# Kernel optimization log

Hardware: AMD Instinct MI355X
Metric: run time of the kernel (lower is better)

## Reference

```python
import jax, jax.numpy as jnp
import numpy as np
from jax import lax

C_OUT, C_IN, KH, KW = 16, 16, 3, 3
STRIDE = (1, 1)
PADDING = ((1, 1), (1, 1))  # symmetric 'same' padding for 3x3, stride 1
DILATION = (1, 1)


def setup_inputs() -> dict:
    key = jax.random.key(0)
    kx, kw = jax.random.split(key)
    x = jax.random.normal(kx, (8, C_IN, 512, 512), dtype=jnp.float32)
    # Conv2DUF stores the conv weight flattened: [out_channels, in_channels*kh*kw]
    weight = jax.random.normal(kw, (C_OUT, C_IN * KH * KW), dtype=jnp.float32) * 0.1
    return {"x": x, "weight": weight}


def reference(x, weight):
    # forward(): F.conv2d(x, weight.reshape(original shape), stride/padding/dilation/groups)
    w = weight.reshape(C_OUT, C_IN, KH, KW)
    out = lax.conv_general_dilated(
        x, w,
        window_strides=STRIDE,
        padding=PADDING,
        rhs_dilation=DILATION,
        dimension_numbers=("NCHW", "OIHW", "NCHW"),
        feature_group_count=1,
    )
    return out  # [8, 16, 512, 512]
```

## Files before the change

kernel.cpp:

```cpp
#include <hip/hip_runtime.h>
#include <hip/hip_bf16.h>


#define IH 512
#define IW 512
#define CI 16
#define CO 16
#define TH 16
#define TW 64
#define LROWS (TH + 2)
#define LCOLS (TW + 2)

typedef short short8  __attribute__((ext_vector_type(8)));
typedef short short4v __attribute__((ext_vector_type(4)));
typedef float f32x4   __attribute__((ext_vector_type(4)));

__device__ __forceinline__ short f32_to_bf16_bits(float v) {
    __hip_bfloat16 b = __float2bfloat16(v);
    return __builtin_bit_cast(short, b);
}

__global__ __launch_bounds__(256, 4)
void conv3x3_mfma(const float* __restrict__ x, const float* __restrict__ wgt,
                  float* __restrict__ out) {
    __shared__ short lds[LROWS * LCOLS * CI];

    const int tid  = threadIdx.x;
    const int wave = tid >> 6;
    const int lane = tid & 63;
    const int quad = lane >> 4;
    const int l15  = lane & 15;

    const int wbase = blockIdx.x * TW;
    const int hbase = blockIdx.y * TH;
    const int n     = blockIdx.z;

    short8 afrag[5];
#pragma unroll
    for (int f = 0; f < 5; ++f) {
#pragma unroll
        for (int j = 0; j < 8; ++j) {
            const int k = f * 32 + quad * 8 + j;
            float val = 0.0f;
            if (k < 144) {
                const int ci  = k & 15;
                const int tap = k >> 4;
                val = wgt[l15 * 144 + ci * 9 + tap];
            }
            afrag[f][j] = f32_to_bf16_bits(val);
        }
    }

    const float* xn = x + (size_t)n * CI * IH * IW;

#pragma unroll
    for (int it = 0; it < 5; ++it) {
        const int i = it * 256 + tid;
        if (it < 4 || i < 1152) {
            const int wseg = i & 15;
            const int cg4  = (i >> 4) & 3;
            const int row  = i >> 6;
            const int gh   = hbase - 1 + row;
            const int gw   = wbase + 4 * wseg;
            short4v pk[4];
            if ((unsigned)gh < (unsigned)IH) {
                f32x4 v[4];
#pragma unroll
                for (int jj = 0; jj < 4; ++jj)
                    v[jj] = *(const f32x4*)(xn + ((size_t)(cg4 * 4 + jj) * IH + gh) * IW + gw);
#pragma unroll
                for (int j = 0; j < 4; ++j)
#pragma unroll
                    for (int jj = 0; jj < 4; ++jj)
                        pk[j][jj] = f32_to_bf16_bits(v[jj][j]);
            } else {
#pragma unroll
                for (int j = 0; j < 4; ++j) pk[j] = (short4v){0, 0, 0, 0};
            }
            const int pbase = row * LCOLS + 1 + 4 * wseg;
#pragma unroll
            for (int k = 0; k < 4; ++k) {
                const int j     = (k + wseg) & 3;
                const int pixel = pbase + j;
                const int slot  = cg4 ^ ((pixel >> 1) & 2);
                *(short4v*)&lds[pixel * 16 + slot * 4] = pk[j];
            }
        }
    }

    if (tid < 144) {
        const int cg4  = tid & 3;
        const int col2 = (tid >> 2) & 1;
        const int row  = tid >> 3;
        const int c    = col2 ? (LCOLS - 1) : 0;
        const int gh   = hbase - 1 + row;
        const int gw   = wbase - 1 + c;
        const bool ok  = ((unsigned)gh < (unsigned)IH) && ((unsigned)gw < (unsigned)IW);
        short4v pk;
#pragma unroll
        for (int j = 0; j < 4; ++j) {
            const float v = ok ? xn[((size_t)(cg4 * 4 + j) * IH + gh) * IW + gw] : 0.0f;
            pk[j] = f32_to_bf16_bits(v);
        }
        const int pixel = row * LCOLS + c;
        const int slot  = cg4 ^ ((pixel >> 1) & 2);
        *(short4v*)&lds[pixel * 16 + slot * 4] = pk;
    }
    __syncthreads();

    const int q = quad & 1;
    int doff[5];
#pragma unroll
    for (int f = 0; f < 5; ++f) {
        const int tap = (f < 4) ? (f * 2 + (quad >> 1)) : 8;
        const int kh  = tap / 3;
        const int kw  = tap - kh * 3;
        doff[f] = kh * LCOLS + kw;
    }

    f32x4 acc[4][4];
#pragma unroll
    for (int r = 0; r < 4; ++r)
#pragma unroll
        for (int c4 = 0; c4 < 4; ++c4)
            acc[r][c4] = (f32x4){0.f, 0.f, 0.f, 0.f};

#pragma unroll
    for (int r = 0; r < 4; ++r) {
        const int hl = wave * 4 + r;
#pragma unroll
        for (int c4 = 0; c4 < 4; ++c4) {
            const int wl    = c4 * 16 + l15;
            const int pbase = hl * LCOLS + wl;
#pragma unroll
            for (int f = 0; f < 5; ++f) {
                const int pixel = pbase + doff[f];
                const int half  = q ^ ((pixel >> 2) & 1);
                const short8 b  = *(const short8*)&lds[pixel * 16 + half * 8];
                acc[r][c4] = __builtin_amdgcn_mfma_f32_16x16x32_bf16(afrag[f], b, acc[r][c4], 0, 0, 0);
            }
        }
    }

    float* on = out + (size_t)n * CO * IH * IW;
#pragma unroll
    for (int r = 0; r < 4; ++r) {
        const int gh = hbase + wave * 4 + r;
#pragma unroll
        for (int c4 = 0; c4 < 4; ++c4) {
            const int gw = wbase + c4 * 16 + l15;
#pragma unroll
            for (int reg = 0; reg < 4; ++reg) {
                const int co = quad * 4 + reg;
                on[((size_t)co * IH + gh) * IW + gw] = acc[r][c4][reg];
            }
        }
    }
}

extern "C" void kernel_launch(void* const* d_in, const int* in_sizes, int n_in,
                              void* d_out, int out_size, void* d_ws, size_t ws_size,
                              hipStream_t stream) {
    const float* x = (const float*)d_in[0];
    const float* w = (const float*)d_in[1];
    float* out     = (float*)d_out;

    dim3 grid(IW / TW, IH / TH, 8);
    dim3 block(256);
    conv3x3_mfma<<<grid, block, 0, stream>>>(x, w, out);
}
```

Baseline: 274.2 us.

## Halve tile width, raise occupancy, and software-pipeline halo loads

Tile width drops from 64 to 32 columns, so each block has half the accumulators and LDS footprint, and launch bounds are raised to 8 blocks per CU. The input staging is split into info/load/store helpers and interleaved so global loads for the next item are issued before earlier items are converted and stored. Weight fragment setup now runs after the loads are issued, which helps hide latency. The cost is more blocks, each with a larger relative halo overhead, so more redundant reads of the halo columns.

```diff
diff --git a/kernel.cpp b/kernel.cpp
--- a/kernel.cpp
+++ b/kernel.cpp
@@ -7,9 +7,10 @@
 #define CI 16
 #define CO 16
 #define TH 16
-#define TW 64
+#define TW 32
 #define LROWS (TH + 2)
 #define LCOLS (TW + 2)
+#define NITEMS (LROWS * (TW / 4) * 4)
 
 typedef short short8  __attribute__((ext_vector_type(8)));
 typedef short short4v __attribute__((ext_vector_type(4)));
@@ -20,7 +21,58 @@
     return __builtin_bit_cast(short, b);
 }
 
-__global__ __launch_bounds__(256, 4)
+struct ItemInfo {
+    const float* src;
+    int pb;
+    int ws;
+    int cg;
+    bool ok;
+};
+
+__device__ __forceinline__ ItemInfo item_info(int i, int hbase, int wbase,
+                                              const float* __restrict__ xn) {
+    ItemInfo t;
+    t.ws = i & 7;
+    t.cg = (i >> 3) & 3;
+    const int row = i >> 5;
+    const int gh  = hbase - 1 + row;
+    t.ok  = (unsigned)gh < (unsigned)IH;
+    t.src = xn + ((size_t)(t.cg * 4) * IH + gh) * IW + (wbase + 4 * t.ws);
+    t.pb  = row * LCOLS + 1 + 4 * t.ws;
+    return t;
+}
+
+__device__ __forceinline__ void item_load(const ItemInfo& t, f32x4 v[4]) {
+    if (t.ok) {
+#pragma unroll
+        for (int jj = 0; jj < 4; ++jj)
+            v[jj] = *(const f32x4*)(t.src + (size_t)jj * IH * IW);
+    }
+}
+
+__device__ __forceinline__ void item_store(const ItemInfo& t, const f32x4 v[4],
+                                           short* lds) {
+    short4v pk[4];
+    if (t.ok) {
+#pragma unroll
+        for (int j = 0; j < 4; ++j)
+#pragma unroll
+            for (int jj = 0; jj < 4; ++jj)
+                pk[j][jj] = f32_to_bf16_bits(v[jj][j]);
+    } else {
+#pragma unroll
+        for (int j = 0; j < 4; ++j) pk[j] = (short4v){0, 0, 0, 0};
+    }
+#pragma unroll
+    for (int k = 0; k < 4; ++k) {
+        const int j     = (k + t.ws) & 3;
+        const int pixel = t.pb + j;
+        const int slot  = t.cg ^ ((pixel >> 1) & 2);
+        *(short4v*)&lds[pixel * 16 + slot * 4] = pk[j];
+    }
+}
+
+__global__ __launch_bounds__(256, 8)
 void conv3x3_mfma(const float* __restrict__ x, const float* __restrict__ wgt,
                   float* __restrict__ out) {
     __shared__ short lds[LROWS * LCOLS * CI];
@@ -34,6 +86,39 @@
     const int wbase = blockIdx.x * TW;
     const int hbase = blockIdx.y * TH;
     const int n     = blockIdx.z;
+
+    const float* xn = x + (size_t)n * CI * IH * IW;
+
+    ItemInfo t0 = item_info(tid,       hbase, wbase, xn);
+    ItemInfo t1 = item_info(tid + 256, hbase, wbase, xn);
+    f32x4 v0[4], v1[4], v2[4];
+    item_load(t0, v0);
+    item_load(t1, v1);
+    const bool has2 = (tid + 512) < NITEMS;
+    ItemInfo t2 = item_info(has2 ? (tid + 512) : tid, hbase, wbase, xn);
+    item_store(t0, v0, lds);
+    if (has2) item_load(t2, v2);
+    item_store(t1, v1, lds);
+    if (has2) item_store(t2, v2, lds);
+
+    if (tid < 144) {
+        const int cg4  = tid & 3;
+        const int col2 = (tid >> 2) & 1;
+        const int row  = tid >> 3;
+        const int c    = col2 ? (LCOLS - 1) : 0;
+        const int gh   = hbase - 1 + row;
+        const int gw   = wbase - 1 + c;
+        const bool ok  = ((unsigned)gh < (unsigned)IH) && ((unsigned)gw < (unsigned)IW);
+        short4v pk;
+#pragma unroll
+        for (int j = 0; j < 4; ++j) {
+            const float v = ok ? xn[((size_t)(cg4 * 4 + j) * IH + gh) * IW + gw] : 0.0f;
+            pk[j] = f32_to_bf16_bits(v);
+        }
+        const int pixel = row * LCOLS + c;
+        const int slot  = cg4 ^ ((pixel >> 1) & 2);
+        *(short4v*)&lds[pixel * 16 + slot * 4] = pk;
+    }
 
     short8 afrag[5];
 #pragma unroll
@@ -50,62 +135,6 @@
             afrag[f][j] = f32_to_bf16_bits(val);
         }
     }
-
-    const float* xn = x + (size_t)n * CI * IH * IW;
-
-#pragma unroll
-    for (int it = 0; it < 5; ++it) {
-        const int i = it * 256 + tid;
-        if (it < 4 || i < 1152) {
-            const int wseg = i & 15;
-            const int cg4  = (i >> 4) & 3;
-            const int row  = i >> 6;
-            const int gh   = hbase - 1 + row;
-            const int gw   = wbase + 4 * wseg;
-            short4v pk[4];
-            if ((unsigned)gh < (unsigned)IH) {
-                f32x4 v[4];
-#pragma unroll
-                for (int jj = 0; jj < 4; ++jj)
-                    v[jj] = *(const f32x4*)(xn + ((size_t)(cg4 * 4 + jj) * IH + gh) * IW + gw);
-#pragma unroll
-                for (int j = 0; j < 4; ++j)
-#pragma unroll
-                    for (int jj = 0; jj < 4; ++jj)
-                        pk[j][jj] = f32_to_bf16_bits(v[jj][j]);
-            } else {
-#pragma unroll
-                for (int j = 0; j < 4; ++j) pk[j] = (short4v){0, 0, 0, 0};
-            }
-            const int pbase = row * LCOLS + 1 + 4 * wseg;
-#pragma unroll
-            for (int k = 0; k < 4; ++k) {
-                const int j     = (k + wseg) & 3;
-                const int pixel = pbase + j;
-                const int slot  = cg4 ^ ((pixel >> 1) & 2);
-                *(short4v*)&lds[pixel * 16 + slot * 4] = pk[j];
-            }
-        }
-    }
-
-    if (tid < 144) {
-        const int cg4  = tid & 3;
-        const int col2 = (tid >> 2) & 1;
-        const int row  = tid >> 3;
-        const int c    = col2 ? (LCOLS - 1) : 0;
-        const int gh   = hbase - 1 + row;
-        const int gw   = wbase - 1 + c;
-        const bool ok  = ((unsigned)gh < (unsigned)IH) && ((unsigned)gw < (unsigned)IW);
-        short4v pk;
-#pragma unroll
-        for (int j = 0; j < 4; ++j) {
-            const float v = ok ? xn[((size_t)(cg4 * 4 + j) * IH + gh) * IW + gw] : 0.0f;
-            pk[j] = f32_to_bf16_bits(v);
-        }
-        const int pixel = row * LCOLS + c;
-        const int slot  = cg4 ^ ((pixel >> 1) & 2);
-        *(short4v*)&lds[pixel * 16 + slot * 4] = pk;
-    }
     __syncthreads();
 
     const int q = quad & 1;
@@ -118,18 +147,18 @@
         doff[f] = kh * LCOLS + kw;
     }
 
-    f32x4 acc[4][4];
+    f32x4 acc[4][2];
 #pragma unroll
     for (int r = 0; r < 4; ++r)
 #pragma unroll
-        for (int c4 = 0; c4 < 4; ++c4)
+        for (int c4 = 0; c4 < 2; ++c4)
             acc[r][c4] = (f32x4){0.f, 0.f, 0.f, 0.f};
 
 #pragma unroll
     for (int r = 0; r < 4; ++r) {
         const int hl = wave * 4 + r;
 #pragma unroll
-        for (int c4 = 0; c4 < 4; ++c4) {
+        for (int c4 = 0; c4 < 2; ++c4) {
             const int wl    = c4 * 16 + l15;
             const int pbase = hl * LCOLS + wl;
 #pragma unroll
@@ -147,7 +176,7 @@
     for (int r = 0; r < 4; ++r) {
         const int gh = hbase + wave * 4 + r;
 #pragma unroll
-        for (int c4 = 0; c4 < 4; ++c4) {
+        for (int c4 = 0; c4 < 2; ++c4) {
             const int gw = wbase + c4 * 16 + l15;
 #pragma unroll
             for (int reg = 0; reg < 4; ++reg) {
```

New measurement: 298.2 us. 8.8% more time.

## Replace LDS-tiled conv with direct global-load MFMA per output row

Applied to the files above, without the earlier changes.

Drops the shared-memory halo tile and builds each MFMA B fragment with scalar global loads straight from the input planes, relying on L1/L2 cache for reuse across the nine taps. Each block now handles one output row of one image, with the batch index interleaved into the block id, and a separate bounds-checked path for edge pixels. This removes the LDS staging and barrier, but each lane issues many strided scalar loads (eight channels per fragment, five fragments) where the old staging used vectorized loads. It also loses the explicit reuse the tile gave across neighbouring rows.

```diff
diff --git a/kernel.cpp b/kernel.cpp
--- a/kernel.cpp
+++ b/kernel.cpp
@@ -6,34 +6,53 @@
 #define IW 512
 #define CI 16
 #define CO 16
-#define TH 16
-#define TW 64
-#define LROWS (TH + 2)
-#define LCOLS (TW + 2)
+#define PLANE (IH * IW)
 
-typedef short short8  __attribute__((ext_vector_type(8)));
-typedef short short4v __attribute__((ext_vector_type(4)));
-typedef float f32x4   __attribute__((ext_vector_type(4)));
+typedef short short8 __attribute__((ext_vector_type(8)));
+typedef float f32x4  __attribute__((ext_vector_type(4)));
 
 __device__ __forceinline__ short f32_to_bf16_bits(float v) {
     __hip_bfloat16 b = __float2bfloat16(v);
     return __builtin_bit_cast(short, b);
 }
 
-__global__ __launch_bounds__(256, 4)
-void conv3x3_mfma(const float* __restrict__ x, const float* __restrict__ wgt,
-                  float* __restrict__ out) {
-    __shared__ short lds[LROWS * LCOLS * CI];
+template<bool SAFE>
+__device__ __forceinline__ short8 build_bfrag(const float* __restrict__ xn,
+                                              int cb, int hh, int ww) {
+    short8 b;
+    if (SAFE) {
+        const int base = cb * PLANE + hh * IW + ww;
+#pragma unroll
+        for (int j = 0; j < 8; ++j)
+            b[j] = f32_to_bf16_bits(xn[base + j * PLANE]);
+    } else {
+        const bool ok = ((unsigned)hh < (unsigned)IH) && ((unsigned)ww < (unsigned)IW);
+        const int hc = ok ? hh : 0;
+        const int wc = ok ? ww : 0;
+        const int base = cb * PLANE + hc * IW + wc;
+#pragma unroll
+        for (int j = 0; j < 8; ++j) {
+            const float v = xn[base + j * PLANE];
+            b[j] = ok ? f32_to_bf16_bits(v) : (short)0;
+        }
+    }
+    return b;
+}
 
+__global__ __launch_bounds__(256, 6)
+void conv3x3_direct(const float* __restrict__ x, const float* __restrict__ wgt,
+                    float* __restrict__ out) {
     const int tid  = threadIdx.x;
     const int wave = tid >> 6;
     const int lane = tid & 63;
     const int quad = lane >> 4;
     const int l15  = lane & 15;
 
-    const int wbase = blockIdx.x * TW;
-    const int hbase = blockIdx.y * TH;
-    const int n     = blockIdx.z;
+    const int bid = blockIdx.x;
+    const int n   = bid & 7;
+    const int h   = bid >> 3;
+
+    const float* xn = x + (size_t)n * CI * PLANE;
 
     short8 afrag[5];
 #pragma unroll
@@ -51,109 +70,43 @@
         }
     }
 
-    const float* xn = x + (size_t)n * CI * IH * IW;
-
-#pragma unroll
-    for (int it = 0; it < 5; ++it) {
-        const int i = it * 256 + tid;
-        if (it < 4 || i < 1152) {
-            const int wseg = i & 15;
-            const int cg4  = (i >> 4) & 3;
-            const int row  = i >> 6;
-            const int gh   = hbase - 1 + row;
-            const int gw   = wbase + 4 * wseg;
-            short4v pk[4];
-            if ((unsigned)gh < (unsigned)IH) {
-                f32x4 v[4];
-#pragma unroll
-                for (int jj = 0; jj < 4; ++jj)
-                    v[jj] = *(const f32x4*)(xn + ((size_t)(cg4 * 4 + jj) * IH + gh) * IW + gw);
-#pragma unroll
-                for (int j = 0; j < 4; ++j)
-#pragma unroll
-                    for (int jj = 0; jj < 4; ++jj)
-                        pk[j][jj] = f32_to_bf16_bits(v[jj][j]);
-            } else {
-#pragma unroll
-                for (int j = 0; j < 4; ++j) pk[j] = (short4v){0, 0, 0, 0};
-            }
-            const int pbase = row * LCOLS + 1 + 4 * wseg;
-#pragma unroll
-            for (int k = 0; k < 4; ++k) {
-                const int j     = (k + wseg) & 3;
-                const int pixel = pbase + j;
-                const int slot  = cg4 ^ ((pixel >> 1) & 2);
-                *(short4v*)&lds[pixel * 16 + slot * 4] = pk[j];
-            }
-        }
-    }
-
-    if (tid < 144) {
-        const int cg4  = tid & 3;
-        const int col2 = (tid >> 2) & 1;
-        const int row  = tid >> 3;
-        const int c    = col2 ? (LCOLS - 1) : 0;
-        const int gh   = hbase - 1 + row;
-        const int gw   = wbase - 1 + c;
-        const bool ok  = ((unsigned)gh < (unsigned)IH) && ((unsigned)gw < (unsigned)IW);
-        short4v pk;
-#pragma unroll
-        for (int j = 0; j < 4; ++j) {
-            const float v = ok ? xn[((size_t)(cg4 * 4 + j) * IH + gh) * IW + gw] : 0.0f;
-            pk[j] = f32_to_bf16_bits(v);
-        }
-        const int pixel = row * LCOLS + c;
-        const int slot  = cg4 ^ ((pixel >> 1) & 2);
-        *(short4v*)&lds[pixel * 16 + slot * 4] = pk;
-    }
-    __syncthreads();
-
-    const int q = quad & 1;
-    int doff[5];
+    const int cb = (quad & 1) * 8;
+    int dh_[5], dw_[5];
 #pragma unroll
     for (int f = 0; f < 5; ++f) {
         const int tap = (f < 4) ? (f * 2 + (quad >> 1)) : 8;
-        const int kh  = tap / 3;
-        const int kw  = tap - kh * 3;
-        doff[f] = kh * LCOLS + kw;
+        dh_[f] = tap / 3 - 1;
+        dw_[f] = tap - (tap / 3) * 3 - 1;
     }
 
-    f32x4 acc[4][4];
-#pragma unroll
-    for (int r = 0; r < 4; ++r)
-#pragma unroll
-        for (int c4 = 0; c4 < 4; ++c4)
-            acc[r][c4] = (f32x4){0.f, 0.f, 0.f, 0.f};
+    const bool hedge = (h == 0) || (h == IH - 1);
+    float* on = out + (size_t)n * CO * PLANE + h * IW;
 
-#pragma unroll
-    for (int r = 0; r < 4; ++r) {
-        const int hl = wave * 4 + r;
-#pragma unroll
-        for (int c4 = 0; c4 < 4; ++c4) {
-            const int wl    = c4 * 16 + l15;
-            const int pbase = hl * LCOLS + wl;
+#pragma unroll 2
+    for (int g = 0; g < 8; ++g) {
+        const int px0 = wave * 128 + g * 16;
+        const bool safe = !hedge && (px0 >= 16) && (px0 <= 480);
+
+        f32x4 acc = (f32x4){0.f, 0.f, 0.f, 0.f};
+        if (safe) {
 #pragma unroll
             for (int f = 0; f < 5; ++f) {
-                const int pixel = pbase + doff[f];
-                const int half  = q ^ ((pixel >> 2) & 1);
-                const short8 b  = *(const short8*)&lds[pixel * 16 + half * 8];
-                acc[r][c4] = __builtin_amdgcn_mfma_f32_16x16x32_bf16(afrag[f], b, acc[r][c4], 0, 0, 0);
+                const short8 b = build_bfrag<true>(xn, cb, h + dh_[f], px0 + l15 + dw_[f]);
+                acc = __builtin_amdgcn_mfma_f32_16x16x32_bf16(afrag[f], b, acc, 0, 0, 0);
+            }
+        } else {
+#pragma unroll
+            for (int f = 0; f < 5; ++f) {
+                const short8 b = build_bfrag<false>(xn, cb, h + dh_[f], px0 + l15 + dw_[f]);
+                acc = __builtin_amdgcn_mfma_f32_16x16x32_bf16(afrag[f], b, acc, 0, 0, 0);
             }
         }
-    }
 
-    float* on = out + (size_t)n * CO * IH * IW;
+        const int gw = px0 + l15;
 #pragma unroll
-    for (int r = 0; r < 4; ++r) {
-        const int gh = hbase + wave * 4 + r;
-#pragma unroll
-        for (int c4 = 0; c4 < 4; ++c4) {
-            const int gw = wbase + c4 * 16 + l15;
-#pragma unroll
-            for (int reg = 0; reg < 4; ++reg) {
-                const int co = quad * 4 + reg;
-                on[((size_t)co * IH + gh) * IW + gw] = acc[r][c4][reg];
-            }
+        for (int reg = 0; reg < 4; ++reg) {
+            const int co = quad * 4 + reg;
+            on[(size_t)co * PLANE + gw] = acc[reg];
         }
     }
 }
@@ -165,7 +118,7 @@
     const float* w = (const float*)d_in[1];
     float* out     = (float*)d_out;
 
-    dim3 grid(IW / TW, IH / TH, 8);
+    dim3 grid(8 * IH);
     dim3 block(256);
-    conv3x3_mfma<<<grid, block, 0, stream>>>(x, w, out);
+    conv3x3_direct<<<grid, block, 0, stream>>>(x, w, out);
 }
```

Result: slower. 430.9 us (+57.2%).
